# Optimization experiments

Measured on AMD Instinct MI355X. Metric: run time of the kernel, lower is better.

Reference implementation:

```python
import jax, jax.numpy as jnp
import numpy as np

B, OBS, T, H = 4096, 16, 32, 512  # batch, encoder length, decode seq_len, hidden_size


def _lstm_cell(x, h, c, Wi, Wh, b):
    # PyTorch gate order: i, f, g, o. b = b_ih + b_hh (mathematically identical).
    g = x @ Wi.T + h @ Wh.T + b
    i, f, gg, o = jnp.split(g, 4, axis=-1)
    c = jax.nn.sigmoid(f) * c + jax.nn.sigmoid(i) * jnp.tanh(gg)
    h = jax.nn.sigmoid(o) * jnp.tanh(c)
    return h, c


def _encode(xs, Wi, Wh, b):
    # xs: [B, T, 4]; returns final (h, c), zero initial state as in nn.LSTM.
    def step(carry, x):
        h, c = _lstm_cell(x, carry[0], carry[1], Wi, Wh, b)
        return (h, c), None
    z = jnp.zeros((xs.shape[0], H), xs.dtype)
    (h, c), _ = jax.lax.scan(step, (z, z), jnp.swapaxes(xs, 0, 1))
    return h, c


def setup_inputs() -> dict:
    key = jax.random.key(0)
    ks = jax.random.split(key, 22)
    s = 0.05
    p = lambda k, shape: (jax.random.normal(k, shape, jnp.float32) * s)
    return {
        "speed": jax.random.normal(ks[0], (B, OBS, 4), jnp.float32),
        "pos": jax.random.normal(ks[1], (B, OBS, 4), jnp.float32),
        "enc_s_Wi": p(ks[2], (4 * H, 4)), "enc_s_Wh": p(ks[3], (4 * H, H)), "enc_s_b": p(ks[4], (4 * H,)),
        "enc_p_Wi": p(ks[5], (4 * H, 4)), "enc_p_Wh": p(ks[6], (4 * H, H)), "enc_p_b": p(ks[7], (4 * H,)),
        "dec_s_Wi": p(ks[8], (4 * H, 4)), "dec_s_Wh": p(ks[9], (4 * H, H)), "dec_s_b": p(ks[10], (4 * H,)),
        "dec_i_Wi": p(ks[11], (4 * H, 4)), "dec_i_Wh": p(ks[12], (4 * H, H)), "dec_i_b": p(ks[13], (4 * H,)),
        "W_fs": p(ks[14], (4, H)), "b_fs": p(ks[15], (4,)),
        "W_fc": p(ks[16], (2, H)), "b_fc": p(ks[17], (2,)),
        "W_emb": p(ks[18], (4, 2)), "b_emb": p(ks[19], (4,)),
    }


def reference(speed, pos,
              enc_s_Wi, enc_s_Wh, enc_s_b,
              enc_p_Wi, enc_p_Wh, enc_p_b,
              dec_s_Wi, dec_s_Wh, dec_s_b,
              dec_i_Wi, dec_i_Wh, dec_i_b,
              W_fs, b_fs, W_fc, b_fc, W_emb, b_emb):
    h_se, c_se = _encode(speed, enc_s_Wi, enc_s_Wh, enc_s_b)
    h_pe, c_pe = _encode(pos, enc_p_Wi, enc_p_Wh, enc_p_b)
    h_s, c_s = h_se + h_pe, c_se + c_pe
    h_i, c_i = h_s, c_s
    last_speed = speed[:, -1, :]
    last_pos = pos[:, -1, :]

    def step(carry, _):
        h_s, c_s, h_i, c_i, ls, lp = carry
        h_s, c_s = _lstm_cell(ls, h_s, c_s, dec_s_Wi, dec_s_Wh, dec_s_b)
        h_i, c_i = _lstm_cell(lp, h_i, c_i, dec_i_Wi, dec_i_Wh, dec_i_b)
        sp = jnp.clip(h_s @ W_fs.T + b_fs, -100.0, 100.0)        # Hardtanh(-100, 100)
        it = jax.nn.relu(h_i @ W_fc.T + b_fc)                     # fc_crossing
        ls = jax.lax.stop_gradient(sp)                            # .detach()
        lp = jax.lax.stop_gradient(jax.nn.relu(it @ W_emb.T + b_emb))  # pos_embedding(.).detach()
        return (h_s, c_s, h_i, c_i, ls, lp), (sp, jax.nn.softmax(it, axis=1))

    carry0 = (h_s, c_s, h_i, c_i, last_speed, last_pos)
    _, (speed_seq, cross_seq) = jax.lax.scan(step, carry0, None, length=T)
    speed_outputs = jnp.swapaxes(speed_seq, 0, 1)   # [B, T, 4]
    # Faithful to the source bug: intention_outputs is never accumulated, so the
    # returned crossing_outputs holds ONLY the last step's softmax: [B, 1, 2].
    crossing_outputs = cross_seq[-1][:, None, :]
    return speed_outputs, crossing_outputs
```

## Files before the change

kernel.cpp:

```cpp
#include <hip/hip_runtime.h>
#include <stdint.h>

#define H 512
#define KAUG 528
#define KT_N 33
#define LROW 536
#define NROW 32
#define WMAT_ELEMS (16 * KT_N * 4 * 512)
#define T_DEC 32
#define B_TOT 4096

typedef __attribute__((ext_vector_type(8))) short short8;
typedef __attribute__((ext_vector_type(16))) float floatx16;

__device__ __forceinline__ unsigned short f2bf(float x) {
  union { float f; unsigned int u; } v; v.f = x;
  unsigned int u = v.u;
  return (unsigned short)((u + 0x7FFFu + ((u >> 16) & 1u)) >> 16);
}
__device__ __forceinline__ float bf2f(unsigned short s) {
  union { unsigned int u; float f; } v; v.u = ((unsigned int)s) << 16;
  return v.f;
}
__device__ __forceinline__ float rcpf(float x) { return __builtin_amdgcn_rcpf(x); }
__device__ __forceinline__ float sigm(float x) { return rcpf(1.0f + __expf(-x)); }
__device__ __forceinline__ float tanh_f(float x) {
  return 1.0f - 2.0f * rcpf(1.0f + __expf(2.0f * x));
}

__global__ void prep_weights(
    const float* __restrict__ Wh_s, const float* __restrict__ Wi_s, const float* __restrict__ b_s,
    const float* __restrict__ Wh_p, const float* __restrict__ Wi_p, const float* __restrict__ b_p,
    const float* __restrict__ Wh_d, const float* __restrict__ Wi_d, const float* __restrict__ b_d,
    const float* __restrict__ Wh_i, const float* __restrict__ Wi_i, const float* __restrict__ b_i,
    short* __restrict__ wpack)
{
  int idx = blockIdx.x * 256 + threadIdx.x;
  const int per = 2048 * KAUG;
  if (idx >= 4 * per) return;
  int mat = idx / per;
  int rem = idx - mat * per;
  int n = rem / KAUG;
  int ka = rem - n * KAUG;
  const float* Wh; const float* Wi; const float* bb;
  if (mat == 0)      { Wh = Wh_s; Wi = Wi_s; bb = b_s; }
  else if (mat == 1) { Wh = Wh_p; Wi = Wi_p; bb = b_p; }
  else if (mat == 2) { Wh = Wh_d; Wi = Wi_d; bb = b_d; }
  else               { Wh = Wh_i; Wi = Wi_i; bb = b_i; }
  float v;
  if (ka < 512)      v = Wh[n * 512 + ka];
  else if (ka < 516) v = Wi[n * 4 + (ka - 512)];
  else if (ka == 516) v = bb[n];
  else               v = 0.0f;
  int g = n >> 9, ntL = (n >> 5) & 15, ni = n & 31;
  int kt = ka >> 4, kh = (ka >> 3) & 1, ks = ka & 7;
  int lanep = kh * 32 + ni;
  wpack[(size_t)mat * WMAT_ELEMS +
        (((((size_t)ntL * KT_N + kt) * 4 + g) << 9) + (lanep << 3) + ks)] = (short)f2bf(v);
}

__device__ __forceinline__ void lstm_step_mfma(
    const short* hl, const short* __restrict__ wm,
    int lane, int wv, float c_reg[2][16], float hnew[2][16])
{
  int arow = lane & 31, ahalf = lane >> 5;
  const short* aptr = hl + arow * LROW + ahalf * 8;
  #pragma unroll
  for (int jt = 0; jt < 2; ++jt) {
    int ntL = wv * 2 + jt;
    const short* bp = wm + (size_t)ntL * (KT_N * 4 * 512) + (lane << 3);
    floatx16 ai = (floatx16)0.0f, af = (floatx16)0.0f, ag = (floatx16)0.0f, ao = (floatx16)0.0f;
    #pragma unroll 3
    for (int kt = 0; kt < KT_N; ++kt) {
      short8 a  = *(const short8*)(aptr + kt * 16);
      short8 b0 = *(const short8*)(bp);
      short8 b1 = *(const short8*)(bp + 512);
      short8 b2 = *(const short8*)(bp + 1024);
      short8 b3 = *(const short8*)(bp + 1536);
      bp += 2048;
      ai = __builtin_amdgcn_mfma_f32_32x32x16_bf16(a, b0, ai, 0, 0, 0);
      af = __builtin_amdgcn_mfma_f32_32x32x16_bf16(a, b1, af, 0, 0, 0);
      ag = __builtin_amdgcn_mfma_f32_32x32x16_bf16(a, b2, ag, 0, 0, 0);
      ao = __builtin_amdgcn_mfma_f32_32x32x16_bf16(a, b3, ao, 0, 0, 0);
    }
    #pragma unroll
    for (int r = 0; r < 16; ++r) {
      float si = sigm(ai[r]);
      float sf = sigm(af[r]);
      float tg = tanh_f(ag[r]);
      float so = sigm(ao[r]);
      float cn = sf * c_reg[jt][r] + si * tg;
      c_reg[jt][r] = cn;
      hnew[jt][r] = so * tanh_f(cn);
    }
  }
}

__device__ __forceinline__ void write_h(short* hl, int lane, int wv, const float hnew[2][16]) {
  int arow = lane & 31, ahalf = lane >> 5;
  #pragma unroll
  for (int jt = 0; jt < 2; ++jt) {
    int col = wv * 64 + jt * 32 + arow;
    #pragma unroll
    for (int r = 0; r < 16; ++r) {
      int row = (r & 3) + ((r >> 2) << 3) + (ahalf << 2);
      hl[row * LROW + col] = (short)f2bf(hnew[jt][r]);
    }
  }
}

__global__ __launch_bounds__(512) void lstm_encoder(
    const float* __restrict__ speed, const float* __restrict__ pos,
    const short* __restrict__ wpack,
    short* __restrict__ h_enc, float* __restrict__ c_enc)
{
  __shared__ short hl[NROW * LROW];
  int tid = threadIdx.x;
  int b = blockIdx.x;
  int xcd = b & 7, slot = b >> 3;
  int enc = xcd >> 2;
  int rg = slot * 4 + (xcd & 3);
  int r0 = rg * 32;
  const float* xin = enc ? pos : speed;
  const short* wm = wpack + (size_t)enc * WMAT_ELEMS;

  for (int i = tid; i < NROW * LROW; i += 512) hl[i] = 0;
  __syncthreads();
  if (tid < 32) hl[tid * LROW + 516] = (short)0x3F80;
  if (tid < 128) {
    int r = tid >> 2, c = tid & 3;
    hl[r * LROW + 512 + c] = (short)f2bf(xin[(r0 + r) * 64 + c]);
  }
  __syncthreads();

  int lane = tid & 63, wv = tid >> 6;
  float c_reg[2][16];
  #pragma unroll
  for (int jt = 0; jt < 2; ++jt)
    #pragma unroll
    for (int r = 0; r < 16; ++r) c_reg[jt][r] = 0.0f;
  float hnew[2][16];

  for (int t = 0; t < 16; ++t) {
    lstm_step_mfma(hl, wm, lane, wv, c_reg, hnew);
    __syncthreads();
    write_h(hl, lane, wv, hnew);
    if (t < 15 && tid < 128) {
      int r = tid >> 2, c = tid & 3;
      hl[r * LROW + 512 + c] = (short)f2bf(xin[(r0 + r) * 64 + (t + 1) * 4 + c]);
    }
    __syncthreads();
  }

  for (int i = tid; i < 32 * 512; i += 512) {
    int r = i >> 9, k = i & 511;
    h_enc[((size_t)(enc * B_TOT + r0 + r) << 9) + k] = hl[r * LROW + k];
  }
  int arow = lane & 31, ahalf = lane >> 5;
  #pragma unroll
  for (int jt = 0; jt < 2; ++jt) {
    int col = wv * 64 + jt * 32 + arow;
    #pragma unroll
    for (int r = 0; r < 16; ++r) {
      int row = (r & 3) + ((r >> 2) << 3) + (ahalf << 2);
      c_enc[((size_t)(enc * B_TOT + r0 + row) << 9) + col] = c_reg[jt][r];
    }
  }
}

__global__ __launch_bounds__(512) void lstm_decoder(
    const float* __restrict__ speed, const float* __restrict__ pos,
    const short* __restrict__ wpack,
    const short* __restrict__ h_enc, const float* __restrict__ c_enc,
    const float* __restrict__ W_fs, const float* __restrict__ b_fs,
    const float* __restrict__ W_fc, const float* __restrict__ b_fc,
    const float* __restrict__ W_emb, const float* __restrict__ b_emb,
    float* __restrict__ out)
{
  __shared__ short hl[NROW * LROW];
  int tid = threadIdx.x;
  int b = blockIdx.x;
  int xcd = b & 7, slot = b >> 3;
  int chain = xcd >> 2;
  int rg = slot * 4 + (xcd & 3);
  int r0 = rg * 32;
  const short* wm = wpack + (size_t)(2 + chain) * WMAT_ELEMS;

  for (int i = tid; i < NROW * LROW; i += 512) hl[i] = 0;
  __syncthreads();
  for (int i = tid; i < 32 * 512; i += 512) {
    int r = i >> 9, k = i & 511;
    float h0 = bf2f((unsigned short)h_enc[((size_t)(r0 + r) << 9) + k])
             + bf2f((unsigned short)h_enc[((size_t)(B_TOT + r0 + r) << 9) + k]);
    hl[r * LROW + k] = (short)f2bf(h0);
  }
  if (tid < 32) hl[tid * LROW + 516] = (short)0x3F80;
  {
    const float* last = chain ? pos : speed;
    if (tid < 128) {
      int r = tid >> 2, c = tid & 3;
      hl[r * LROW + 512 + c] = (short)f2bf(last[(r0 + r) * 64 + 60 + c]);
    }
  }
  int lane = tid & 63, wv = tid >> 6;
  int arow = lane & 31, ahalf = lane >> 5;
  float c_reg[2][16];
  #pragma unroll
  for (int jt = 0; jt < 2; ++jt) {
    int col = wv * 64 + jt * 32 + arow;
    #pragma unroll
    for (int r = 0; r < 16; ++r) {
      int row = (r & 3) + ((r >> 2) << 3) + (ahalf << 2);
      size_t gi = ((size_t)(r0 + row) << 9) + col;
      c_reg[jt][r] = c_enc[gi] + c_enc[gi + (((size_t)B_TOT) << 9)];
    }
  }
  __syncthreads();

  float wro[4][8];
  float hb[4];
  float we[8], be[4];
  if (chain == 0) {
    #pragma unroll
    for (int o = 0; o < 4; ++o) {
      #pragma unroll
      for (int j = 0; j < 8; ++j) wro[o][j] = W_fs[o * 512 + lane * 8 + j];
      hb[o] = b_fs[o];
    }
  } else {
    #pragma unroll
    for (int o = 0; o < 2; ++o) {
      #pragma unroll
      for (int j = 0; j < 8; ++j) wro[o][j] = W_fc[o * 512 + lane * 8 + j];
      hb[o] = b_fc[o];
    }
    #pragma unroll
    for (int j = 0; j < 8; ++j) we[j] = W_emb[j];
    #pragma unroll
    for (int o = 0; o < 4; ++o) be[o] = b_emb[o];
  }

  float hnew[2][16];
  for (int t = 0; t < T_DEC; ++t) {
    lstm_step_mfma(hl, wm, lane, wv, c_reg, hnew);
    __syncthreads();
    write_h(hl, lane, wv, hnew);
    __syncthreads();
    #pragma unroll 1
    for (int r = 0; r < 4; ++r) {
      int row = wv * 4 + r;
      const short8 hvs = *(const short8*)(hl + row * LROW + lane * 8);
      float hv[8];
      #pragma unroll
      for (int j = 0; j < 8; ++j) hv[j] = bf2f((unsigned short)hvs[j]);
      if (chain == 0) {
        float p0 = 0.f, p1 = 0.f, p2 = 0.f, p3 = 0.f;
        #pragma unroll
        for (int j = 0; j < 8; ++j) {
          p0 += hv[j] * wro[0][j];
          p1 += hv[j] * wro[1][j];
          p2 += hv[j] * wro[2][j];
          p3 += hv[j] * wro[3][j];
        }
        #pragma unroll
        for (int off = 32; off > 0; off >>= 1) {
          p0 += __shfl_xor(p0, off);
          p1 += __shfl_xor(p1, off);
          p2 += __shfl_xor(p2, off);
          p3 += __shfl_xor(p3, off);
        }
        float s0 = fminf(fmaxf(p0 + hb[0], -100.0f), 100.0f);
        float s1 = fminf(fmaxf(p1 + hb[1], -100.0f), 100.0f);
        float s2 = fminf(fmaxf(p2 + hb[2], -100.0f), 100.0f);
        float s3 = fminf(fmaxf(p3 + hb[3], -100.0f), 100.0f);
        if (lane < 4) {
          float v = (lane == 0) ? s0 : (lane == 1) ? s1 : (lane == 2) ? s2 : s3;
          out[(size_t)(r0 + row) * 128 + t * 4 + lane] = v;
          hl[row * LROW + 512 + lane] = (short)f2bf(v);
        }
      } else {
        float p0 = 0.f, p1 = 0.f;
        #pragma unroll
        for (int j = 0; j < 8; ++j) {
          p0 += hv[j] * wro[0][j];
          p1 += hv[j] * wro[1][j];
        }
        #pragma unroll
        for (int off = 32; off > 0; off >>= 1) {
          p0 += __shfl_xor(p0, off);
          p1 += __shfl_xor(p1, off);
        }
        float it0 = fmaxf(p0 + hb[0], 0.0f);
        float it1 = fmaxf(p1 + hb[1], 0.0f);
        if (lane < 4) {
          float lp = fmaxf(we[lane * 2] * it0 + we[lane * 2 + 1] * it1 + be[lane], 0.0f);
          hl[row * LROW + 512 + lane] = (short)f2bf(lp);
        }
        if (t == T_DEC - 1 && lane < 2) {
          float m = fmaxf(it0, it1);
          float e0 = __expf(it0 - m), e1 = __expf(it1 - m);
          float v = ((lane == 0) ? e0 : e1) * rcpf(e0 + e1);
          out[(size_t)524288 + (size_t)(r0 + row) * 2 + lane] = v;
        }
      }
    }
    __syncthreads();
  }
}

extern "C" void kernel_launch(void* const* d_in, const int* in_sizes, int n_in,
                              void* d_out, int out_size, void* d_ws, size_t ws_size,
                              hipStream_t stream)
{
  const float* speed    = (const float*)d_in[0];
  const float* pos      = (const float*)d_in[1];
  const float* enc_s_Wi = (const float*)d_in[2];
  const float* enc_s_Wh = (const float*)d_in[3];
  const float* enc_s_b  = (const float*)d_in[4];
  const float* enc_p_Wi = (const float*)d_in[5];
  const float* enc_p_Wh = (const float*)d_in[6];
  const float* enc_p_b  = (const float*)d_in[7];
  const float* dec_s_Wi = (const float*)d_in[8];
  const float* dec_s_Wh = (const float*)d_in[9];
  const float* dec_s_b  = (const float*)d_in[10];
  const float* dec_i_Wi = (const float*)d_in[11];
  const float* dec_i_Wh = (const float*)d_in[12];
  const float* dec_i_b  = (const float*)d_in[13];
  const float* W_fs     = (const float*)d_in[14];
  const float* b_fs     = (const float*)d_in[15];
  const float* W_fc     = (const float*)d_in[16];
  const float* b_fc     = (const float*)d_in[17];
  const float* W_emb    = (const float*)d_in[18];
  const float* b_emb    = (const float*)d_in[19];
  float* out = (float*)d_out;

  char* ws = (char*)d_ws;
  short* wpack = (short*)ws;
  short* h_enc = (short*)(ws + 8650752);
  float* c_enc = (float*)(ws + 17039360);

  prep_weights<<<16896, 256, 0, stream>>>(
      enc_s_Wh, enc_s_Wi, enc_s_b,
      enc_p_Wh, enc_p_Wi, enc_p_b,
      dec_s_Wh, dec_s_Wi, dec_s_b,
      dec_i_Wh, dec_i_Wi, dec_i_b,
      wpack);
  lstm_encoder<<<256, 512, 0, stream>>>(speed, pos, wpack, h_enc, c_enc);
  lstm_decoder<<<256, 512, 0, stream>>>(speed, pos, wpack, h_enc, c_enc,
                                        W_fs, b_fs, W_fc, b_fc, W_emb, b_emb, out);
}
```

Baseline: 1.328 ms.

## Split LSTM gate tiles across 16 waves with 1024-thread blocks

Doubles the workgroup to 1024 threads so each of 16 waves computes one 32-column gate tile instead of two, halving per-wave MFMA work and register state. The decoder's head projection is redistributed to two rows per wave, and the head weights are read from global memory inside the loop instead of being held in registers. This aims for more latency hiding and parallelism within a CU per timestep. The cost is lower register budget per thread under launch_bounds(1024) and repeated global loads of the head weights every step.

```diff
diff --git a/kernel.cpp b/kernel.cpp
--- a/kernel.cpp
+++ b/kernel.cpp
@@ -61,55 +61,48 @@
 
 __device__ __forceinline__ void lstm_step_mfma(
     const short* hl, const short* __restrict__ wm,
-    int lane, int wv, float c_reg[2][16], float hnew[2][16])
+    int lane, int wv, float c_reg[16], float hnew[16])
 {
   int arow = lane & 31, ahalf = lane >> 5;
   const short* aptr = hl + arow * LROW + ahalf * 8;
+  const short* bp = wm + (size_t)wv * (KT_N * 4 * 512) + (lane << 3);
+  floatx16 ai = (floatx16)0.0f, af = (floatx16)0.0f, ag = (floatx16)0.0f, ao = (floatx16)0.0f;
+  #pragma unroll 3
+  for (int kt = 0; kt < KT_N; ++kt) {
+    short8 a  = *(const short8*)(aptr + kt * 16);
+    short8 b0 = *(const short8*)(bp);
+    short8 b1 = *(const short8*)(bp + 512);
+    short8 b2 = *(const short8*)(bp + 1024);
+    short8 b3 = *(const short8*)(bp + 1536);
+    bp += 2048;
+    ai = __builtin_amdgcn_mfma_f32_32x32x16_bf16(a, b0, ai, 0, 0, 0);
+    af = __builtin_amdgcn_mfma_f32_32x32x16_bf16(a, b1, af, 0, 0, 0);
+    ag = __builtin_amdgcn_mfma_f32_32x32x16_bf16(a, b2, ag, 0, 0, 0);
+    ao = __builtin_amdgcn_mfma_f32_32x32x16_bf16(a, b3, ao, 0, 0, 0);
+  }
   #pragma unroll
-  for (int jt = 0; jt < 2; ++jt) {
-    int ntL = wv * 2 + jt;
-    const short* bp = wm + (size_t)ntL * (KT_N * 4 * 512) + (lane << 3);
-    floatx16 ai = (floatx16)0.0f, af = (floatx16)0.0f, ag = (floatx16)0.0f, ao = (floatx16)0.0f;
-    #pragma unroll 3
-    for (int kt = 0; kt < KT_N; ++kt) {
-      short8 a  = *(const short8*)(aptr + kt * 16);
-      short8 b0 = *(const short8*)(bp);
-      short8 b1 = *(const short8*)(bp + 512);
-      short8 b2 = *(const short8*)(bp + 1024);
-      short8 b3 = *(const short8*)(bp + 1536);
-      bp += 2048;
-      ai = __builtin_amdgcn_mfma_f32_32x32x16_bf16(a, b0, ai, 0, 0, 0);
-      af = __builtin_amdgcn_mfma_f32_32x32x16_bf16(a, b1, af, 0, 0, 0);
-      ag = __builtin_amdgcn_mfma_f32_32x32x16_bf16(a, b2, ag, 0, 0, 0);
-      ao = __builtin_amdgcn_mfma_f32_32x32x16_bf16(a, b3, ao, 0, 0, 0);
-    }
-    #pragma unroll
-    for (int r = 0; r < 16; ++r) {
-      float si = sigm(ai[r]);
-      float sf = sigm(af[r]);
-      float tg = tanh_f(ag[r]);
-      float so = sigm(ao[r]);
-      float cn = sf * c_reg[jt][r] + si * tg;
-      c_reg[jt][r] = cn;
-      hnew[jt][r] = so * tanh_f(cn);
-    }
-  }
-}
-
-__device__ __forceinline__ void write_h(short* hl, int lane, int wv, const float hnew[2][16]) {
+  for (int r = 0; r < 16; ++r) {
+    float si = sigm(ai[r]);
+    float sf = sigm(af[r]);
+    float tg = tanh_f(ag[r]);
+    float so = sigm(ao[r]);
+    float cn = sf * c_reg[r] + si * tg;
+    c_reg[r] = cn;
+    hnew[r] = so * tanh_f(cn);
+  }
+}
+
+__device__ __forceinline__ void write_h(short* hl, int lane, int wv, const float hnew[16]) {
   int arow = lane & 31, ahalf = lane >> 5;
+  int col = (wv << 5) + arow;
   #pragma unroll
-  for (int jt = 0; jt < 2; ++jt) {
-    int col = wv * 64 + jt * 32 + arow;
-    #pragma unroll
-    for (int r = 0; r < 16; ++r) {
-      int row = (r & 3) + ((r >> 2) << 3) + (ahalf << 2);
-      hl[row * LROW + col] = (short)f2bf(hnew[jt][r]);
-    }
-  }
-}
-
-__global__ __launch_bounds__(512) void lstm_encoder(
+  for (int r = 0; r < 16; ++r) {
+    int row = (r & 3) + ((r >> 2) << 3) + (ahalf << 2);
+    hl[row * LROW + col] = (short)f2bf(hnew[r]);
+  }
+}
+
+__global__ __launch_bounds__(1024) void lstm_encoder(
     const float* __restrict__ speed, const float* __restrict__ pos,
     const short* __restrict__ wpack,
     short* __restrict__ h_enc, float* __restrict__ c_enc)
@@ -124,7 +117,7 @@
   const float* xin = enc ? pos : speed;
   const short* wm = wpack + (size_t)enc * WMAT_ELEMS;
 
-  for (int i = tid; i < NROW * LROW; i += 512) hl[i] = 0;
+  for (int i = tid; i < NROW * LROW; i += 1024) hl[i] = 0;
   __syncthreads();
   if (tid < 32) hl[tid * LROW + 516] = (short)0x3F80;
   if (tid < 128) {
@@ -134,12 +127,10 @@
   __syncthreads();
 
   int lane = tid & 63, wv = tid >> 6;
-  float c_reg[2][16];
+  float c_reg[16];
   #pragma unroll
-  for (int jt = 0; jt < 2; ++jt)
-    #pragma unroll
-    for (int r = 0; r < 16; ++r) c_reg[jt][r] = 0.0f;
-  float hnew[2][16];
+  for (int r = 0; r < 16; ++r) c_reg[r] = 0.0f;
+  float hnew[16];
 
   for (int t = 0; t < 16; ++t) {
     lstm_step_mfma(hl, wm, lane, wv, c_reg, hnew);
@@ -152,23 +143,20 @@
     __syncthreads();
   }
 
-  for (int i = tid; i < 32 * 512; i += 512) {
+  for (int i = tid; i < 32 * 512; i += 1024) {
     int r = i >> 9, k = i & 511;
     h_enc[((size_t)(enc * B_TOT + r0 + r) << 9) + k] = hl[r * LROW + k];
   }
   int arow = lane & 31, ahalf = lane >> 5;
+  int col = (wv << 5) + arow;
   #pragma unroll
-  for (int jt = 0; jt < 2; ++jt) {
-    int col = wv * 64 + jt * 32 + arow;
-    #pragma unroll
-    for (int r = 0; r < 16; ++r) {
-      int row = (r & 3) + ((r >> 2) << 3) + (ahalf << 2);
-      c_enc[((size_t)(enc * B_TOT + r0 + row) << 9) + col] = c_reg[jt][r];
-    }
-  }
-}
-
-__global__ __launch_bounds__(512) void lstm_decoder(
+  for (int r = 0; r < 16; ++r) {
+    int row = (r & 3) + ((r >> 2) << 3) + (ahalf << 2);
+    c_enc[((size_t)(enc * B_TOT + r0 + row) << 9) + col] = c_reg[r];
+  }
+}
+
+__global__ __launch_bounds__(1024) void lstm_decoder(
     const float* __restrict__ speed, const float* __restrict__ pos,
     const short* __restrict__ wpack,
     const short* __restrict__ h_enc, const float* __restrict__ c_enc,
@@ -186,9 +174,9 @@
   int r0 = rg * 32;
   const short* wm = wpack + (size_t)(2 + chain) * WMAT_ELEMS;
 
-  for (int i = tid; i < NROW * LROW; i += 512) hl[i] = 0;
+  for (int i = tid; i < NROW * LROW; i += 1024) hl[i] = 0;
   __syncthreads();
-  for (int i = tid; i < 32 * 512; i += 512) {
+  for (int i = tid; i < 32 * 512; i += 1024) {
     int r = i >> 9, k = i & 511;
     float h0 = bf2f((unsigned short)h_enc[((size_t)(r0 + r) << 9) + k])
              + bf2f((unsigned short)h_enc[((size_t)(B_TOT + r0 + r) << 9) + k]);
@@ -204,51 +192,26 @@
   }
   int lane = tid & 63, wv = tid >> 6;
   int arow = lane & 31, ahalf = lane >> 5;
-  float c_reg[2][16];
-  #pragma unroll
-  for (int jt = 0; jt < 2; ++jt) {
-    int col = wv * 64 + jt * 32 + arow;
+  float c_reg[16];
+  {
+    int col = (wv << 5) + arow;
     #pragma unroll
     for (int r = 0; r < 16; ++r) {
       int row = (r & 3) + ((r >> 2) << 3) + (ahalf << 2);
       size_t gi = ((size_t)(r0 + row) << 9) + col;
-      c_reg[jt][r] = c_enc[gi] + c_enc[gi + (((size_t)B_TOT) << 9)];
+      c_reg[r] = c_enc[gi] + c_enc[gi + (((size_t)B_TOT) << 9)];
     }
   }
   __syncthreads();
 
-  float wro[4][8];
-  float hb[4];
-  float we[8], be[4];
-  if (chain == 0) {
-    #pragma unroll
-    for (int o = 0; o < 4; ++o) {
-      #pragma unroll
-      for (int j = 0; j < 8; ++j) wro[o][j] = W_fs[o * 512 + lane * 8 + j];
-      hb[o] = b_fs[o];
-    }
-  } else {
-    #pragma unroll
-    for (int o = 0; o < 2; ++o) {
-      #pragma unroll
-      for (int j = 0; j < 8; ++j) wro[o][j] = W_fc[o * 512 + lane * 8 + j];
-      hb[o] = b_fc[o];
-    }
-    #pragma unroll
-    for (int j = 0; j < 8; ++j) we[j] = W_emb[j];
-    #pragma unroll
-    for (int o = 0; o < 4; ++o) be[o] = b_emb[o];
-  }
-
-  float hnew[2][16];
+  float hnew[16];
   for (int t = 0; t < T_DEC; ++t) {
     lstm_step_mfma(hl, wm, lane, wv, c_reg, hnew);
     __syncthreads();
     write_h(hl, lane, wv, hnew);
     __syncthreads();
-    #pragma unroll 1
-    for (int r = 0; r < 4; ++r) {
-      int row = wv * 4 + r;
+    for (int r = 0; r < 2; ++r) {
+      int row = wv * 2 + r;
       const short8 hvs = *(const short8*)(hl + row * LROW + lane * 8);
       float hv[8];
       #pragma unroll
@@ -257,10 +220,10 @@
         float p0 = 0.f, p1 = 0.f, p2 = 0.f, p3 = 0.f;
         #pragma unroll
         for (int j = 0; j < 8; ++j) {
-          p0 += hv[j] * wro[0][j];
-          p1 += hv[j] * wro[1][j];
-          p2 += hv[j] * wro[2][j];
-          p3 += hv[j] * wro[3][j];
+          p0 += hv[j] * W_fs[0 * 512 + lane * 8 + j];
+          p1 += hv[j] * W_fs[1 * 512 + lane * 8 + j];
+          p2 += hv[j] * W_fs[2 * 512 + lane * 8 + j];
+          p3 += hv[j] * W_fs[3 * 512 + lane * 8 + j];
         }
         #pragma unroll
         for (int off = 32; off > 0; off >>= 1) {
@@ -269,10 +232,10 @@
           p2 += __shfl_xor(p2, off);
           p3 += __shfl_xor(p3, off);
         }
-        float s0 = fminf(fmaxf(p0 + hb[0], -100.0f), 100.0f);
-        float s1 = fminf(fmaxf(p1 + hb[1], -100.0f), 100.0f);
-        float s2 = fminf(fmaxf(p2 + hb[2], -100.0f), 100.0f);
-        float s3 = fminf(fmaxf(p3 + hb[3], -100.0f), 100.0f);
+        float s0 = fminf(fmaxf(p0 + b_fs[0], -100.0f), 100.0f);
+        float s1 = fminf(fmaxf(p1 + b_fs[1], -100.0f), 100.0f);
+        float s2 = fminf(fmaxf(p2 + b_fs[2], -100.0f), 100.0f);
+        float s3 = fminf(fmaxf(p3 + b_fs[3], -100.0f), 100.0f);
         if (lane < 4) {
           float v = (lane == 0) ? s0 : (lane == 1) ? s1 : (lane == 2) ? s2 : s3;
           out[(size_t)(r0 + row) * 128 + t * 4 + lane] = v;
@@ -282,18 +245,18 @@
         float p0 = 0.f, p1 = 0.f;
         #pragma unroll
         for (int j = 0; j < 8; ++j) {
-          p0 += hv[j] * wro[0][j];
-          p1 += hv[j] * wro[1][j];
+          p0 += hv[j] * W_fc[0 * 512 + lane * 8 + j];
+          p1 += hv[j] * W_fc[1 * 512 + lane * 8 + j];
         }
         #pragma unroll
         for (int off = 32; off > 0; off >>= 1) {
           p0 += __shfl_xor(p0, off);
           p1 += __shfl_xor(p1, off);
         }
-        float it0 = fmaxf(p0 + hb[0], 0.0f);
-        float it1 = fmaxf(p1 + hb[1], 0.0f);
+        float it0 = fmaxf(p0 + b_fc[0], 0.0f);
+        float it1 = fmaxf(p1 + b_fc[1], 0.0f);
         if (lane < 4) {
-          float lp = fmaxf(we[lane * 2] * it0 + we[lane * 2 + 1] * it1 + be[lane], 0.0f);
+          float lp = fmaxf(W_emb[lane * 2] * it0 + W_emb[lane * 2 + 1] * it1 + b_emb[lane], 0.0f);
           hl[row * LROW + 512 + lane] = (short)f2bf(lp);
         }
         if (t == T_DEC - 1 && lane < 2) {
@@ -345,7 +308,7 @@
       dec_s_Wh, dec_s_Wi, dec_s_b,
       dec_i_Wh, dec_i_Wi, dec_i_b,
       wpack);
-  lstm_encoder<<<256, 512, 0, stream>>>(speed, pos, wpack, h_enc, c_enc);
-  lstm_decoder<<<256, 512, 0, stream>>>(speed, pos, wpack, h_enc, c_enc,
-                                        W_fs, b_fs, W_fc, b_fc, W_emb, b_emb, out);
-}
+  lstm_encoder<<<256, 1024, 0, stream>>>(speed, pos, wpack, h_enc, c_enc);
+  lstm_decoder<<<256, 1024, 0, stream>>>(speed, pos, wpack, h_enc, c_enc,
+                                         W_fs, b_fs, W_fc, b_fc, W_emb, b_emb, out);
+}
```

Measured after the change: 1.249 ms. -5.9%, faster.

## Double-buffer LSTM hidden state, widen encoder to 1024 threads, fp32 decoder input path

Applied to the files above, without the earlier changes.

The encoder now runs 16 waves per block, each owning one 32-column tile, and ping-pongs the hidden state between two LDS buffers so each step needs one barrier instead of two. The decoder also double-buffers h, drops the augmented K tile (33 to 32 k-steps), and adds the 4-wide input projection and bias in fp32 registers from an LDS x buffer. It fuses the h write into the gate epilogue. This cuts barriers and MFMA work but raises register and LDS use per block.

```diff
diff --git a/kernel.cpp b/kernel.cpp
--- a/kernel.cpp
+++ b/kernel.cpp
@@ -27,6 +27,8 @@
 __device__ __forceinline__ float tanh_f(float x) {
   return 1.0f - 2.0f * rcpf(1.0f + __expf(2.0f * x));
 }
+
+#define MFMA(A, B, C) __builtin_amdgcn_mfma_f32_32x32x16_bf16(A, B, C, 0, 0, 0)
 
 __global__ void prep_weights(
     const float* __restrict__ Wh_s, const float* __restrict__ Wi_s, const float* __restrict__ b_s,
@@ -61,60 +63,51 @@
 
 __device__ __forceinline__ void lstm_step_mfma(
     const short* hl, const short* __restrict__ wm,
-    int lane, int wv, float c_reg[2][16], float hnew[2][16])
+    int lane, int wv, float c_reg[16], float hnew[16])
 {
   int arow = lane & 31, ahalf = lane >> 5;
   const short* aptr = hl + arow * LROW + ahalf * 8;
-  #pragma unroll
-  for (int jt = 0; jt < 2; ++jt) {
-    int ntL = wv * 2 + jt;
-    const short* bp = wm + (size_t)ntL * (KT_N * 4 * 512) + (lane << 3);
-    floatx16 ai = (floatx16)0.0f, af = (floatx16)0.0f, ag = (floatx16)0.0f, ao = (floatx16)0.0f;
-    #pragma unroll 3
-    for (int kt = 0; kt < KT_N; ++kt) {
-      short8 a  = *(const short8*)(aptr + kt * 16);
-      short8 b0 = *(const short8*)(bp);
-      short8 b1 = *(const short8*)(bp + 512);
-      short8 b2 = *(const short8*)(bp + 1024);
-      short8 b3 = *(const short8*)(bp + 1536);
-      bp += 2048;
-      ai = __builtin_amdgcn_mfma_f32_32x32x16_bf16(a, b0, ai, 0, 0, 0);
-      af = __builtin_amdgcn_mfma_f32_32x32x16_bf16(a, b1, af, 0, 0, 0);
-      ag = __builtin_amdgcn_mfma_f32_32x32x16_bf16(a, b2, ag, 0, 0, 0);
-      ao = __builtin_amdgcn_mfma_f32_32x32x16_bf16(a, b3, ao, 0, 0, 0);
-    }
-    #pragma unroll
-    for (int r = 0; r < 16; ++r) {
-      float si = sigm(ai[r]);
-      float sf = sigm(af[r]);
-      float tg = tanh_f(ag[r]);
-      float so = sigm(ao[r]);
-      float cn = sf * c_reg[jt][r] + si * tg;
-      c_reg[jt][r] = cn;
-      hnew[jt][r] = so * tanh_f(cn);
-    }
-  }
-}
-
-__device__ __forceinline__ void write_h(short* hl, int lane, int wv, const float hnew[2][16]) {
+  const short* bp = wm + (size_t)wv * (KT_N * 4 * 512) + (lane << 3);
+  floatx16 ai = (floatx16)0.0f, af = (floatx16)0.0f, ag = (floatx16)0.0f, ao = (floatx16)0.0f;
+  #pragma unroll 3
+  for (int kt = 0; kt < KT_N; ++kt) {
+    short8 a  = *(const short8*)(aptr + kt * 16);
+    short8 b0 = *(const short8*)(bp);
+    short8 b1 = *(const short8*)(bp + 512);
+    short8 b2 = *(const short8*)(bp + 1024);
+    short8 b3 = *(const short8*)(bp + 1536);
+    bp += 2048;
+    ai = MFMA(a, b0, ai); af = MFMA(a, b1, af);
+    ag = MFMA(a, b2, ag); ao = MFMA(a, b3, ao);
+  }
+  #pragma unroll
+  for (int r = 0; r < 16; ++r) {
+    float si = sigm(ai[r]);
+    float sf = sigm(af[r]);
+    float tg = tanh_f(ag[r]);
+    float so = sigm(ao[r]);
+    float cn = sf * c_reg[r] + si * tg;
+    c_reg[r] = cn;
+    hnew[r] = so * tanh_f(cn);
+  }
+}
+
+__device__ __forceinline__ void write_h16(short* hl, int lane, int wv, const float hnew[16]) {
   int arow = lane & 31, ahalf = lane >> 5;
-  #pragma unroll
-  for (int jt = 0; jt < 2; ++jt) {
-    int col = wv * 64 + jt * 32 + arow;
-    #pragma unroll
-    for (int r = 0; r < 16; ++r) {
-      int row = (r & 3) + ((r >> 2) << 3) + (ahalf << 2);
-      hl[row * LROW + col] = (short)f2bf(hnew[jt][r]);
-    }
-  }
-}
-
-__global__ __launch_bounds__(512) void lstm_encoder(
+  int col = (wv << 5) + arow;
+  #pragma unroll
+  for (int r = 0; r < 16; ++r) {
+    int row = (r & 3) + ((r >> 2) << 3) + (ahalf << 2);
+    hl[row * LROW + col] = (short)f2bf(hnew[r]);
+  }
+}
+
+__global__ __launch_bounds__(1024) void lstm_encoder(
     const float* __restrict__ speed, const float* __restrict__ pos,
     const short* __restrict__ wpack,
     short* __restrict__ h_enc, float* __restrict__ c_enc)
 {
-  __shared__ short hl[NROW * LROW];
+  __shared__ short hl[2][NROW * LROW];
   int tid = threadIdx.x;
   int b = blockIdx.x;
   int xcd = b & 7, slot = b >> 3;
@@ -124,60 +117,62 @@
   const float* xin = enc ? pos : speed;
   const short* wm = wpack + (size_t)enc * WMAT_ELEMS;
 
-  for (int i = tid; i < NROW * LROW; i += 512) hl[i] = 0;
+  {
+    short* hz = &hl[0][0];
+    for (int i = tid; i < 2 * NROW * LROW; i += 1024) hz[i] = 0;
+  }
   __syncthreads();
-  if (tid < 32) hl[tid * LROW + 516] = (short)0x3F80;
+  if (tid < 64) hl[tid >> 5][(tid & 31) * LROW + 516] = (short)0x3F80;
   if (tid < 128) {
     int r = tid >> 2, c = tid & 3;
-    hl[r * LROW + 512 + c] = (short)f2bf(xin[(r0 + r) * 64 + c]);
+    hl[0][r * LROW + 512 + c] = (short)f2bf(xin[(r0 + r) * 64 + c]);
   }
   __syncthreads();
 
   int lane = tid & 63, wv = tid >> 6;
-  float c_reg[2][16];
-  #pragma unroll
-  for (int jt = 0; jt < 2; ++jt)
-    #pragma unroll
-    for (int r = 0; r < 16; ++r) c_reg[jt][r] = 0.0f;
-  float hnew[2][16];
+  float c_reg[16];
+  #pragma unroll
+  for (int r = 0; r < 16; ++r) c_reg[r] = 0.0f;
+  float hnew[16];
 
   for (int t = 0; t < 16; ++t) {
-    lstm_step_mfma(hl, wm, lane, wv, c_reg, hnew);
-    __syncthreads();
-    write_h(hl, lane, wv, hnew);
+    const short* cb = hl[t & 1];
+    short* nb = &hl[(t + 1) & 1][0];
+    lstm_step_mfma(cb, wm, lane, wv, c_reg, hnew);
+    write_h16(nb, lane, wv, hnew);
     if (t < 15 && tid < 128) {
       int r = tid >> 2, c = tid & 3;
-      hl[r * LROW + 512 + c] = (short)f2bf(xin[(r0 + r) * 64 + (t + 1) * 4 + c]);
+      nb[r * LROW + 512 + c] = (short)f2bf(xin[(r0 + r) * 64 + (t + 1) * 4 + c]);
     }
     __syncthreads();
   }
 
-  for (int i = tid; i < 32 * 512; i += 512) {
+  for (int i = tid; i < 32 * 512; i += 1024) {
     int r = i >> 9, k = i & 511;
-    h_enc[((size_t)(enc * B_TOT + r0 + r) << 9) + k] = hl[r * LROW + k];
+    h_enc[((size_t)(enc * B_TOT + r0 + r) << 9) + k] = hl[0][r * LROW + k];
   }
   int arow = lane & 31, ahalf = lane >> 5;
-  #pragma unroll
-  for (int jt = 0; jt < 2; ++jt) {
-    int col = wv * 64 + jt * 32 + arow;
-    #pragma unroll
-    for (int r = 0; r < 16; ++r) {
-      int row = (r & 3) + ((r >> 2) << 3) + (ahalf << 2);
-      c_enc[((size_t)(enc * B_TOT + r0 + row) << 9) + col] = c_reg[jt][r];
-    }
+  int col = (wv << 5) + arow;
+  #pragma unroll
+  for (int r = 0; r < 16; ++r) {
+    int row = (r & 3) + ((r >> 2) << 3) + (ahalf << 2);
+    c_enc[((size_t)(enc * B_TOT + r0 + row) << 9) + col] = c_reg[r];
   }
 }
 
 __global__ __launch_bounds__(512) void lstm_decoder(
     const float* __restrict__ speed, const float* __restrict__ pos,
     const short* __restrict__ wpack,
+    const float* __restrict__ dWi_s, const float* __restrict__ db_s,
+    const float* __restrict__ dWi_i, const float* __restrict__ db_i,
     const short* __restrict__ h_enc, const float* __restrict__ c_enc,
     const float* __restrict__ W_fs, const float* __restrict__ b_fs,
     const float* __restrict__ W_fc, const float* __restrict__ b_fc,
     const float* __restrict__ W_emb, const float* __restrict__ b_emb,
     float* __restrict__ out)
 {
-  __shared__ short hl[NROW * LROW];
+  __shared__ short hl[2][NROW * LROW];
+  __shared__ float xs[2][32][4];
   int tid = threadIdx.x;
   int b = blockIdx.x;
   int xcd = b & 7, slot = b >> 3;
@@ -185,25 +180,23 @@
   int rg = slot * 4 + (xcd & 3);
   int r0 = rg * 32;
   const short* wm = wpack + (size_t)(2 + chain) * WMAT_ELEMS;
-
-  for (int i = tid; i < NROW * LROW; i += 512) hl[i] = 0;
-  __syncthreads();
+  int lane = tid & 63, wv = tid >> 6;
+  int arow = lane & 31, ahalf = lane >> 5;
+
   for (int i = tid; i < 32 * 512; i += 512) {
     int r = i >> 9, k = i & 511;
     float h0 = bf2f((unsigned short)h_enc[((size_t)(r0 + r) << 9) + k])
              + bf2f((unsigned short)h_enc[((size_t)(B_TOT + r0 + r) << 9) + k]);
-    hl[r * LROW + k] = (short)f2bf(h0);
-  }
-  if (tid < 32) hl[tid * LROW + 516] = (short)0x3F80;
+    hl[0][r * LROW + k] = (short)f2bf(h0);
+  }
   {
     const float* last = chain ? pos : speed;
     if (tid < 128) {
       int r = tid >> 2, c = tid & 3;
-      hl[r * LROW + 512 + c] = (short)f2bf(last[(r0 + r) * 64 + 60 + c]);
-    }
-  }
-  int lane = tid & 63, wv = tid >> 6;
-  int arow = lane & 31, ahalf = lane >> 5;
+      xs[0][r][c] = last[(r0 + r) * 64 + 60 + c];
+    }
+  }
+
   float c_reg[2][16];
   #pragma unroll
   for (int jt = 0; jt < 2; ++jt) {
@@ -215,11 +208,23 @@
       c_reg[jt][r] = c_enc[gi] + c_enc[gi + (((size_t)B_TOT) << 9)];
     }
   }
-  __syncthreads();
-
-  float wro[4][8];
-  float hb[4];
-  float we[8], be[4];
+
+  const float* dWi = chain ? dWi_i : dWi_s;
+  const float* dbv = chain ? db_i  : db_s;
+  float wx[2][4][4], wb[2][4];
+  #pragma unroll
+  for (int jt = 0; jt < 2; ++jt) {
+    int col = wv * 64 + jt * 32 + arow;
+    #pragma unroll
+    for (int g = 0; g < 4; ++g) {
+      int n = g * 512 + col;
+      #pragma unroll
+      for (int c = 0; c < 4; ++c) wx[jt][g][c] = dWi[n * 4 + c];
+      wb[jt][g] = dbv[n];
+    }
+  }
+
+  float wro[4][8], hb[4], we[8], be[4];
   if (chain == 0) {
     #pragma unroll
     for (int o = 0; o < 4; ++o) {
@@ -239,17 +244,52 @@
     #pragma unroll
     for (int o = 0; o < 4; ++o) be[o] = b_emb[o];
   }
-
-  float hnew[2][16];
+  __syncthreads();
+
   for (int t = 0; t < T_DEC; ++t) {
-    lstm_step_mfma(hl, wm, lane, wv, c_reg, hnew);
+    const short* cb = hl[t & 1];
+    short* nb = &hl[(t + 1) & 1][0];
+    const float (*xr)[4] = xs[t & 1];
+    float (*xw)[4] = xs[(t + 1) & 1];
+
+    const short* aptr = cb + arow * LROW + ahalf * 8;
+    #pragma unroll
+    for (int jt = 0; jt < 2; ++jt) {
+      int ntL = wv * 2 + jt;
+      const short* bp = wm + (size_t)ntL * (KT_N * 4 * 512) + (lane << 3);
+      floatx16 ai = (floatx16)0.0f, af = (floatx16)0.0f,
+               ag = (floatx16)0.0f, ao = (floatx16)0.0f;
+      #pragma unroll 2
+      for (int kt = 0; kt < 32; ++kt) {
+        short8 a  = *(const short8*)(aptr + kt * 16);
+        short8 b0 = *(const short8*)(bp);
+        short8 b1 = *(const short8*)(bp + 512);
+        short8 b2 = *(const short8*)(bp + 1024);
+        short8 b3 = *(const short8*)(bp + 1536);
+        bp += 2048;
+        ai = MFMA(a, b0, ai); af = MFMA(a, b1, af);
+        ag = MFMA(a, b2, ag); ao = MFMA(a, b3, ao);
+      }
+      int col = wv * 64 + jt * 32 + arow;
+      #pragma unroll
+      for (int r = 0; r < 16; ++r) {
+        int row = (r & 3) + ((r >> 2) << 3) + (ahalf << 2);
+        float x0 = xr[row][0], x1 = xr[row][1], x2 = xr[row][2], x3 = xr[row][3];
+        float gi = ai[r] + wb[jt][0] + wx[jt][0][0]*x0 + wx[jt][0][1]*x1 + wx[jt][0][2]*x2 + wx[jt][0][3]*x3;
+        float gf = af[r] + wb[jt][1] + wx[jt][1][0]*x0 + wx[jt][1][1]*x1 + wx[jt][1][2]*x2 + wx[jt][1][3]*x3;
+        float gg = ag[r] + wb[jt][2] + wx[jt][2][0]*x0 + wx[jt][2][1]*x1 + wx[jt][2][2]*x2 + wx[jt][2][3]*x3;
+        float go = ao[r] + wb[jt][3] + wx[jt][3][0]*x0 + wx[jt][3][1]*x1 + wx[jt][3][2]*x2 + wx[jt][3][3]*x3;
+        float cn = sigm(gf) * c_reg[jt][r] + sigm(gi) * tanh_f(gg);
+        c_reg[jt][r] = cn;
+        nb[row * LROW + col] = (short)f2bf(sigm(go) * tanh_f(cn));
+      }
+    }
     __syncthreads();
-    write_h(hl, lane, wv, hnew);
-    __syncthreads();
+
     #pragma unroll 1
     for (int r = 0; r < 4; ++r) {
       int row = wv * 4 + r;
-      const short8 hvs = *(const short8*)(hl + row * LROW + lane * 8);
+      const short8 hvs = *(const short8*)(nb + row * LROW + lane * 8);
       float hv[8];
       #pragma unroll
       for (int j = 0; j < 8; ++j) hv[j] = bf2f((unsigned short)hvs[j]);
@@ -276,7 +316,7 @@
         if (lane < 4) {
           float v = (lane == 0) ? s0 : (lane == 1) ? s1 : (lane == 2) ? s2 : s3;
           out[(size_t)(r0 + row) * 128 + t * 4 + lane] = v;
-          hl[row * LROW + 512 + lane] = (short)f2bf(v);
+          xw[row][lane] = v;
         }
       } else {
         float p0 = 0.f, p1 = 0.f;
@@ -294,7 +334,7 @@
         float it1 = fmaxf(p1 + hb[1], 0.0f);
         if (lane < 4) {
           float lp = fmaxf(we[lane * 2] * it0 + we[lane * 2 + 1] * it1 + be[lane], 0.0f);
-          hl[row * LROW + 512 + lane] = (short)f2bf(lp);
+          xw[row][lane] = lp;
         }
         if (t == T_DEC - 1 && lane < 2) {
           float m = fmaxf(it0, it1);
@@ -345,7 +385,9 @@
       dec_s_Wh, dec_s_Wi, dec_s_b,
       dec_i_Wh, dec_i_Wi, dec_i_b,
       wpack);
-  lstm_encoder<<<256, 512, 0, stream>>>(speed, pos, wpack, h_enc, c_enc);
-  lstm_decoder<<<256, 512, 0, stream>>>(speed, pos, wpack, h_enc, c_enc,
+  lstm_encoder<<<256, 1024, 0, stream>>>(speed, pos, wpack, h_enc, c_enc);
+  lstm_decoder<<<256, 512, 0, stream>>>(speed, pos, wpack,
+                                        dec_s_Wi, dec_s_b, dec_i_Wi, dec_i_b,
+                                        h_enc, c_enc,
                                         W_fs, b_fs, W_fc, b_fc, W_emb, b_emb, out);
 }
```

New measurement: 1.315 ms. Within noise of the previous version (-1.0%).
